# Optimization experiments

Measured on AMD Instinct MI355X. Metric: run time of the kernel, lower is better.

Reference implementation:

```python
import jax, jax.numpy as jnp
import numpy as np

H = 50  # hidden size

def _lstm_last_h(x, W_ih, W_hh, b_ih, b_hh):
    """Run a single-layer LSTM (PyTorch gate order i,f,g,o) over x [B,T,1],
    return final hidden state h_T [B,H]. Zero initial (h, c)."""
    B = x.shape[0]
    h0 = jnp.zeros((B, H), dtype=x.dtype)
    c0 = jnp.zeros((B, H), dtype=x.dtype)
    b = b_ih + b_hh  # [4H]

    def step(carry, xt):
        h, c = carry
        # gates: [B,4H]
        gates = xt @ W_ih.T + h @ W_hh.T + b
        i, f, g, o = jnp.split(gates, 4, axis=-1)
        i = jax.nn.sigmoid(i)
        f = jax.nn.sigmoid(f)
        g = jnp.tanh(g)
        o = jax.nn.sigmoid(o)
        c = f * c + i * g
        h = o * jnp.tanh(c)
        return (h, c), None

    xt = jnp.swapaxes(x, 0, 1)  # [T,B,1]
    (hT, _), _ = jax.lax.scan(step, (h0, c0), xt)
    return hT


def setup_inputs() -> dict:
    key = jax.random.key(0)
    ks = jax.random.split(key, 7)
    B, T = 1024, 96
    s = 1.0 / np.sqrt(H)  # PyTorch LSTM init scale
    return {
        "x": jax.random.normal(ks[0], (B, T, 1), dtype=jnp.float32),
        "W_ih": jax.random.uniform(ks[1], (4 * H, 1), jnp.float32, -s, s),
        "W_hh": jax.random.uniform(ks[2], (4 * H, H), jnp.float32, -s, s),
        "b_ih": jax.random.uniform(ks[3], (4 * H,), jnp.float32, -s, s),
        "b_hh": jax.random.uniform(ks[4], (4 * H,), jnp.float32, -s, s),
        "W_fc": jax.random.uniform(ks[5], (1, H), jnp.float32, -s, s),
        "b_fc": jax.random.uniform(ks[6], (1,), jnp.float32, -s, s),
        "num_pred": 12,
    }


def reference(x, W_ih, W_hh, b_ih, b_hh, W_fc, b_fc, num_pred):
    preds = []
    for _ in range(num_pred):  # static loop over prediction horizon
        hT = _lstm_last_h(x, W_ih, W_hh, b_ih, b_hh)        # [B,H]
        out = hT @ W_fc.T + b_fc                            # [B,1]
        preds.append(out[:, 0])
        # append prediction as next input, drop oldest timestep (window slides)
        x = jnp.concatenate([x, out[:, :, None]], axis=1)[:, 1:, :]
    return jnp.stack(preds, axis=1)  # [B, num_pred]
```

## Files before the change

kernel.cpp:

```cpp
#include <hip/hip_runtime.h>
#include <stdint.h>


#define HSZ 50
#define TLEN 96

#define GRP(WT,A0,A1,A2,A3,IL,IH,FL,FH,GL,GH,OL,OH,BL,BH,POST) \
    "s_waitcnt lgkmcnt(" WT ")\n\t" \
    "v_pk_fma_f32 v[" A0 "], v[" IL "], v[" BL "], v[" A0 "]\n\t" \
    "v_pk_fma_f32 v[" A1 "], v[" FL "], v[" BL "], v[" A1 "]\n\t" \
    "v_pk_fma_f32 v[" A2 "], v[" GL "], v[" BL "], v[" A2 "]\n\t" \
    "v_pk_fma_f32 v[" A3 "], v[" OL "], v[" BL "], v[" A3 "]\n\t" \
    "v_pk_fma_f32 v[" A0 "], v[" IH "], v[" BH "], v[" A0 "]\n\t" \
    "v_pk_fma_f32 v[" A1 "], v[" FH "], v[" BH "], v[" A1 "]\n\t" \
    "v_pk_fma_f32 v[" A2 "], v[" GH "], v[" BH "], v[" A2 "]\n\t" \
    "v_pk_fma_f32 v[" A3 "], v[" OH "], v[" BH "], v[" A3 "]\n\t" \
    POST
#define GRPM(WT,A0,A1,A2,A3,IL,IH,FL,FH,GL,GH,OL,OH,BL,BH,POST) \
    "s_waitcnt lgkmcnt(" WT ")\n\t" \
    "v_pk_mul_f32 v[" A0 "], v[" IL "], v[" BL "]\n\t" \
    "v_pk_mul_f32 v[" A1 "], v[" FL "], v[" BL "]\n\t" \
    "v_pk_mul_f32 v[" A2 "], v[" GL "], v[" BL "]\n\t" \
    "v_pk_mul_f32 v[" A3 "], v[" OL "], v[" BL "]\n\t" \
    "v_pk_fma_f32 v[" A0 "], v[" IH "], v[" BH "], v[" A0 "]\n\t" \
    "v_pk_fma_f32 v[" A1 "], v[" FH "], v[" BH "], v[" A1 "]\n\t" \
    "v_pk_fma_f32 v[" A2 "], v[" GH "], v[" BH "], v[" A2 "]\n\t" \
    "v_pk_fma_f32 v[" A3 "], v[" OH "], v[" BH "], v[" A3 "]\n\t" \
    POST
#define GRPX(...)  GRP(__VA_ARGS__)
#define GRPMX(...) GRPM(__VA_ARGS__)

#define ACC "28:29","30:31","32:33","34:35"
#define W0  "48:49","50:51","100:101","102:103","152:153","154:155","204:205","206:207"
#define W1  "52:53","54:55","104:105","106:107","156:157","158:159","208:209","210:211"
#define W2  "56:57","58:59","108:109","110:111","160:161","162:163","212:213","214:215"
#define W3  "60:61","62:63","112:113","114:115","164:165","166:167","216:217","218:219"
#define W4  "64:65","66:67","116:117","118:119","168:169","170:171","220:221","222:223"
#define W5  "68:69","70:71","120:121","122:123","172:173","174:175","224:225","226:227"
#define W6  "72:73","74:75","124:125","126:127","176:177","178:179","228:229","230:231"
#define W7  "76:77","78:79","128:129","130:131","180:181","182:183","232:233","234:235"
#define W8  "80:81","82:83","132:133","134:135","184:185","186:187","236:237","238:239"
#define W9  "84:85","86:87","136:137","138:139","188:189","190:191","240:241","242:243"
#define W10 "88:89","90:91","140:141","142:143","192:193","194:195","244:245","246:247"
#define W11 "92:93","94:95","144:145","146:147","196:197","198:199","248:249","250:251"
#define W12 "96:97","98:99","148:149","150:151","200:201","202:203","252:253","254:255"
#define SL0 "0:1","2:3"
#define SL1 "4:5","6:7"
#define SL2 "8:9","10:11"
#define SL3 "12:13","14:15"
#define SL4 "16:17","18:19"
#define SL5 "20:21","22:23"
#define SL6 "24:25","26:27"

__global__ __attribute__((amdgpu_flat_work_group_size(64, 64),
                          amdgpu_waves_per_eu(1, 1)))
void rec_lstm_kernel(const float* __restrict__ x,
                     const float* __restrict__ W_ih,
                     const float* __restrict__ W_hh,
                     const float* __restrict__ b_ih,
                     const float* __restrict__ b_hh,
                     const float* __restrict__ W_fc,
                     const float* __restrict__ b_fc,
                     const int*   __restrict__ num_pred,
                     float*       __restrict__ out)
{
    const int b = blockIdx.x;
    const int j = threadIdx.x;

    __shared__ __align__(16) float lds[176];
    if (j < 48) { lds[64 + j] = x[b*TLEN + j]; lds[64 + j + 48] = x[b*TLEN + j + 48]; }

    const int NP = num_pred[0];
    const uint32_t lb = (uint32_t)(uintptr_t)&lds[0];

    asm volatile(
        "s_load_dword s25, %[bfcp], 0x0\n\t"
        "s_waitcnt lgkmcnt(0)\n\t"
        "v_mbcnt_lo_u32_b32 v0, -1, 0\n\t"
        "v_mbcnt_hi_u32_b32 v0, -1, v0\n\t"
        "s_mov_b32 s22, 49\n\t"
        "v_min_u32 v1, s22, v0\n\t"
        "s_mov_b32 s22, 200\n\t"
        "v_mul_lo_u32 v2, s22, v1\n\t"
        "s_mov_b32 s22, 10000\n\t"
        "v_add_u32 v3, s22, v2\n\t"
        "s_mov_b32 s22, 20000\n\t"
        "v_add_u32 v4, s22, v2\n\t"
        "s_mov_b32 s22, 30000\n\t"
        "v_add_u32 v5, s22, v2\n\t"
        "v_lshlrev_b32 v6, 2, v1\n\t"
        "global_load_dword v48,  v6, %[bih]\n\t"
        "global_load_dword v100, v6, %[bih] offset:200\n\t"
        "global_load_dword v152, v6, %[bih] offset:400\n\t"
        "global_load_dword v204, v6, %[bih] offset:600\n\t"
        "global_load_dword v7,  v6, %[bhh]\n\t"
        "global_load_dword v8,  v6, %[bhh] offset:200\n\t"
        "global_load_dword v9,  v6, %[bhh] offset:400\n\t"
        "global_load_dword v10, v6, %[bhh] offset:600\n\t"
        "global_load_dword v49,  v6, %[wih]\n\t"
        "global_load_dword v101, v6, %[wih] offset:200\n\t"
        "global_load_dword v153, v6, %[wih] offset:400\n\t"
        "global_load_dword v205, v6, %[wih] offset:600\n\t"
        "global_load_dword v41, v6, %[wfcp]\n\t"
        "global_load_dwordx4 v[50:53], v2, %[whh]\n\t"
        "global_load_dwordx4 v[54:57], v2, %[whh] offset:16\n\t"
        "global_load_dwordx4 v[58:61], v2, %[whh] offset:32\n\t"
        "global_load_dwordx4 v[62:65], v2, %[whh] offset:48\n\t"
        "global_load_dwordx4 v[66:69], v2, %[whh] offset:64\n\t"
        "global_load_dwordx4 v[70:73], v2, %[whh] offset:80\n\t"
        "global_load_dwordx4 v[74:77], v2, %[whh] offset:96\n\t"
        "global_load_dwordx4 v[78:81], v2, %[whh] offset:112\n\t"
        "global_load_dwordx4 v[82:85], v2, %[whh] offset:128\n\t"
        "global_load_dwordx4 v[86:89], v2, %[whh] offset:144\n\t"
        "global_load_dwordx4 v[90:93], v2, %[whh] offset:160\n\t"
        "global_load_dwordx4 v[94:97], v2, %[whh] offset:176\n\t"
        "global_load_dwordx2 v[98:99], v2, %[whh] offset:192\n\t"
        "global_load_dwordx4 v[102:105], v3, %[whh]\n\t"
        "global_load_dwordx4 v[106:109], v3, %[whh] offset:16\n\t"
        "global_load_dwordx4 v[110:113], v3, %[whh] offset:32\n\t"
        "global_load_dwordx4 v[114:117], v3, %[whh] offset:48\n\t"
        "global_load_dwordx4 v[118:121], v3, %[whh] offset:64\n\t"
        "global_load_dwordx4 v[122:125], v3, %[whh] offset:80\n\t"
        "global_load_dwordx4 v[126:129], v3, %[whh] offset:96\n\t"
        "global_load_dwordx4 v[130:133], v3, %[whh] offset:112\n\t"
        "global_load_dwordx4 v[134:137], v3, %[whh] offset:128\n\t"
        "global_load_dwordx4 v[138:141], v3, %[whh] offset:144\n\t"
        "global_load_dwordx4 v[142:145], v3, %[whh] offset:160\n\t"
        "global_load_dwordx4 v[146:149], v3, %[whh] offset:176\n\t"
        "global_load_dwordx2 v[150:151], v3, %[whh] offset:192\n\t"
        "global_load_dwordx4 v[154:157], v4, %[whh]\n\t"
        "global_load_dwordx4 v[158:161], v4, %[whh] offset:16\n\t"
        "global_load_dwordx4 v[162:165], v4, %[whh] offset:32\n\t"
        "global_load_dwordx4 v[166:169], v4, %[whh] offset:48\n\t"
        "global_load_dwordx4 v[170:173], v4, %[whh] offset:64\n\t"
        "global_load_dwordx4 v[174:177], v4, %[whh] offset:80\n\t"
        "global_load_dwordx4 v[178:181], v4, %[whh] offset:96\n\t"
        "global_load_dwordx4 v[182:185], v4, %[whh] offset:112\n\t"
        "global_load_dwordx4 v[186:189], v4, %[whh] offset:128\n\t"
        "global_load_dwordx4 v[190:193], v4, %[whh] offset:144\n\t"
        "global_load_dwordx4 v[194:197], v4, %[whh] offset:160\n\t"
        "global_load_dwordx4 v[198:201], v4, %[whh] offset:176\n\t"
        "global_load_dwordx2 v[202:203], v4, %[whh] offset:192\n\t"
        "global_load_dwordx4 v[206:209], v5, %[whh]\n\t"
        "global_load_dwordx4 v[210:213], v5, %[whh] offset:16\n\t"
        "global_load_dwordx4 v[214:217], v5, %[whh] offset:32\n\t"
        "global_load_dwordx4 v[218:221], v5, %[whh] offset:48\n\t"
        "global_load_dwordx4 v[222:225], v5, %[whh] offset:64\n\t"
        "global_load_dwordx4 v[226:229], v5, %[whh] offset:80\n\t"
        "global_load_dwordx4 v[230:233], v5, %[whh] offset:96\n\t"
        "global_load_dwordx4 v[234:237], v5, %[whh] offset:112\n\t"
        "global_load_dwordx4 v[238:241], v5, %[whh] offset:128\n\t"
        "global_load_dwordx4 v[242:245], v5, %[whh] offset:144\n\t"
        "global_load_dwordx4 v[246:249], v5, %[whh] offset:160\n\t"
        "global_load_dwordx4 v[250:253], v5, %[whh] offset:176\n\t"
        "global_load_dwordx2 v[254:255], v5, %[whh] offset:192\n\t"
        "s_waitcnt vmcnt(0)\n\t"
        "v_add_f32 v48,  v48,  v7\n\t"
        "v_add_f32 v100, v100, v8\n\t"
        "v_add_f32 v152, v152, v9\n\t"
        "v_add_f32 v204, v204, v10\n\t"
        "v_cmp_gt_u32 vcc, 50, v0\n\t"
        "v_cndmask_b32 v41, 0, v41, vcc\n\t"
        "v_mov_b32 v38, %[lb]\n\t"
        "v_lshl_add_u32 v39, v1, 2, v38\n\t"
        "v_add_u32 v39, 8, v39\n\t"
        "v_add_u32 v40, 0x100, v38\n\t"
        "v_mov_b32 v44, 1.0\n\t"
        "ds_write_b32 v38, v44\n\t"
        "s_mov_b32 s21, %[np]\n\t"
        "4:\n\t"
        "v_mov_b32 v36, 0\n\t"
        "v_mov_b32 v44, 0\n\t"
        "ds_write_b32 v39, v44\n\t"
        "ds_read_b32 v42, v40\n\t"
        "s_waitcnt lgkmcnt(0)\n\t"
        "ds_write_b32 v38, v42 offset:4\n\t"
        "ds_read_b128 v[0:3],   v38 offset:0\n\t"
        "ds_read_b128 v[4:7],   v38 offset:16\n\t"
        "ds_read_b128 v[8:11],  v38 offset:32\n\t"
        "ds_read_b128 v[12:15], v38 offset:48\n\t"
        "ds_read_b128 v[16:19], v38 offset:64\n\t"
        "ds_read_b128 v[20:23], v38 offset:80\n\t"
        "ds_read_b128 v[24:27], v38 offset:96\n\t"
        "s_mov_b32 s20, 96\n\t"
        "3:\n\t"
        "ds_read_b32 v42, v40 offset:4\n\t"
        GRPMX("7", ACC, W0,  SL0, "ds_read_b128 v[0:3],   v38 offset:112\n\t")
        GRPX("7",  ACC, W1,  SL1, "ds_read_b128 v[4:7],   v38 offset:128\n\t")
        GRPX("7",  ACC, W2,  SL2, "ds_read_b128 v[8:11],  v38 offset:144\n\t")
        GRPX("7",  ACC, W3,  SL3, "ds_read_b128 v[12:15], v38 offset:160\n\t")
        GRPX("7",  ACC, W4,  SL4, "ds_read_b128 v[16:19], v38 offset:176\n\t")
        GRPX("7",  ACC, W5,  SL5, "ds_read_b128 v[20:23], v38 offset:192\n\t")
        GRPX("7",  ACC, W6,  SL6, "")
        GRPX("5",  ACC, W7,  SL0, "")
        GRPX("4",  ACC, W8,  SL1, "")
        GRPX("3",  ACC, W9,  SL2, "")
        GRPX("2",  ACC, W10, SL3, "")
        GRPX("1",  ACC, W11, SL4, "")
        GRPX("0",  ACC, W12, SL5, "")
        "v_add_f32 v28, v28, v29\n\t"
        "v_add_f32 v30, v30, v31\n\t"
        "v_add_f32 v32, v32, v33\n\t"
        "v_add_f32 v34, v34, v35\n\t"
        "v_mul_f32 v29, 0xbfb8aa3b, v28\n\t"
        "v_mul_f32 v31, 0xbfb8aa3b, v30\n\t"
        "v_mul_f32 v33, 0x4038aa3b, v32\n\t"
        "v_mul_f32 v35, 0xbfb8aa3b, v34\n\t"
        "v_exp_f32 v29, v29\n\t"
        "v_exp_f32 v31, v31\n\t"
        "v_exp_f32 v33, v33\n\t"
        "v_exp_f32 v35, v35\n\t"
        "v_add_f32 v29, 1.0, v29\n\t"
        "v_add_f32 v31, 1.0, v31\n\t"
        "v_add_f32 v33, 1.0, v33\n\t"
        "v_add_f32 v35, 1.0, v35\n\t"
        "v_rcp_f32 v29, v29\n\t"
        "v_rcp_f32 v31, v31\n\t"
        "v_rcp_f32 v33, v33\n\t"
        "v_rcp_f32 v35, v35\n\t"
        "s_nop 1\n\t"
        "v_fma_f32 v33, -2.0, v33, 1.0\n\t"
        "v_mul_f32 v29, v29, v33\n\t"
        "v_fma_f32 v36, v31, v36, v29\n\t"
        "v_mul_f32 v31, 0x4038aa3b, v36\n\t"
        "v_exp_f32 v31, v31\n\t"
        "s_nop 1\n\t"
        "v_add_f32 v31, 1.0, v31\n\t"
        "v_rcp_f32 v31, v31\n\t"
        "s_nop 1\n\t"
        "v_fma_f32 v31, -2.0, v31, 1.0\n\t"
        "v_mul_f32 v37, v35, v31\n\t"
        "ds_write_b32 v39, v37\n\t"
        "ds_write_b32 v38, v42 offset:4\n\t"
        "ds_read_b128 v[0:3],   v38 offset:0\n\t"
        "ds_read_b128 v[4:7],   v38 offset:16\n\t"
        "ds_read_b128 v[8:11],  v38 offset:32\n\t"
        "ds_read_b128 v[12:15], v38 offset:48\n\t"
        "ds_read_b128 v[16:19], v38 offset:64\n\t"
        "ds_read_b128 v[20:23], v38 offset:80\n\t"
        "ds_read_b128 v[24:27], v38 offset:96\n\t"
        "v_add_u32 v40, 4, v40\n\t"
        "s_sub_u32 s20, s20, 1\n\t"
        "s_cmp_lg_u32 s20, 0\n\t"
        "s_cbranch_scc1 3b\n\t"
        "v_mul_f32 v44, v37, v41\n\t"
        "s_nop 1\n\t"
        "ds_swizzle_b32 v45, v44 offset:0x041F\n\t"
        "s_waitcnt lgkmcnt(0)\n\t"
        "v_add_f32 v44, v44, v45\n\t"
        "ds_swizzle_b32 v45, v44 offset:0x081F\n\t"
        "s_waitcnt lgkmcnt(0)\n\t"
        "v_add_f32 v44, v44, v45\n\t"
        "ds_swizzle_b32 v45, v44 offset:0x101F\n\t"
        "s_waitcnt lgkmcnt(0)\n\t"
        "v_add_f32 v44, v44, v45\n\t"
        "ds_swizzle_b32 v45, v44 offset:0x201F\n\t"
        "s_waitcnt lgkmcnt(0)\n\t"
        "v_add_f32 v44, v44, v45\n\t"
        "ds_swizzle_b32 v45, v44 offset:0x401F\n\t"
        "s_waitcnt lgkmcnt(0)\n\t"
        "v_add_f32 v44, v44, v45\n\t"
        "s_nop 1\n\t"
        "v_readlane_b32 s26, v44, 0\n\t"
        "v_readlane_b32 s27, v44, 32\n\t"
        "s_nop 4\n\t"
        "v_mov_b32 v45, s26\n\t"
        "v_add_f32 v45, s27, v45\n\t"
        "v_add_f32 v45, s25, v45\n\t"
        "ds_write_b32 v40, v45\n\t"
        "s_waitcnt lgkmcnt(0)\n\t"
        "v_add_u32 v40, 0xfffffe84, v40\n\t"
        "s_sub_u32 s21, s21, 1\n\t"
        "s_cmp_lg_u32 s21, 0\n\t"
        "s_cbranch_scc1 4b\n\t"
        :
        : [lb] "v"(lb), [np] "s"(NP),
          [whh] "s"(W_hh), [wih] "s"(W_ih), [bih] "s"(b_ih), [bhh] "s"(b_hh),
          [wfcp] "s"(W_fc), [bfcp] "s"(b_fc)
        : "memory", "scc", "vcc", "s20", "s21", "s22", "s25", "s26", "s27",
          "v0","v1","v2","v3","v4","v5","v6","v7","v8","v9","v10","v11",
          "v12","v13","v14","v15","v16","v17","v18","v19","v20","v21","v22",
          "v23","v24","v25","v26","v27","v28","v29","v30","v31","v32","v33",
          "v34","v35","v36","v37","v38","v39","v40","v41","v42","v43","v44",
          "v45",
          "v48","v49","v50","v51","v52","v53","v54","v55","v56","v57","v58",
          "v59","v60","v61","v62","v63","v64","v65","v66","v67","v68","v69",
          "v70","v71","v72","v73","v74","v75","v76","v77","v78","v79","v80",
          "v81","v82","v83","v84","v85","v86","v87","v88","v89","v90","v91",
          "v92","v93","v94","v95","v96","v97","v98","v99","v100","v101",
          "v102","v103","v104","v105","v106","v107","v108","v109","v110",
          "v111","v112","v113","v114","v115","v116","v117","v118","v119",
          "v120","v121","v122","v123","v124","v125","v126","v127","v128",
          "v129","v130","v131","v132","v133","v134","v135","v136","v137",
          "v138","v139","v140","v141","v142","v143","v144","v145","v146",
          "v147","v148","v149","v150","v151","v152","v153","v154","v155",
          "v156","v157","v158","v159","v160","v161","v162","v163","v164",
          "v165","v166","v167","v168","v169","v170","v171","v172","v173",
          "v174","v175","v176","v177","v178","v179","v180","v181","v182",
          "v183","v184","v185","v186","v187","v188","v189","v190","v191",
          "v192","v193","v194","v195","v196","v197","v198","v199","v200",
          "v201","v202","v203","v204","v205","v206","v207","v208","v209",
          "v210","v211","v212","v213","v214","v215","v216","v217","v218",
          "v219","v220","v221","v222","v223","v224","v225","v226","v227",
          "v228","v229","v230","v231","v232","v233","v234","v235","v236",
          "v237","v238","v239","v240","v241","v242","v243","v244","v245",
          "v246","v247","v248","v249","v250","v251","v252","v253","v254",
          "v255");

    if (j < NP) out[b * NP + j] = lds[64 + TLEN + j];
}

extern "C" void kernel_launch(void* const* d_in, const int* in_sizes, int n_in,
                              void* d_out, int out_size, void* d_ws, size_t ws_size,
                              hipStream_t stream)
{
    const float* x    = (const float*)d_in[0];
    const float* W_ih = (const float*)d_in[1];
    const float* W_hh = (const float*)d_in[2];
    const float* b_ih = (const float*)d_in[3];
    const float* b_hh = (const float*)d_in[4];
    const float* W_fc = (const float*)d_in[5];
    const float* b_fc = (const float*)d_in[6];
    const int*   np   = (const int*)d_in[7];
    float* out = (float*)d_out;

    const int B = in_sizes[0] / TLEN;
    rec_lstm_kernel<<<B, 64, 0, stream>>>(x, W_ih, W_hh, b_ih, b_hh,
                                          W_fc, b_fc, np, out);
}
```

Baseline: 501.4 us.

## Pipeline alternating prediction horizons across two waves with LDS flag handoff

Launches two waves per block. Each wave handles every other prediction of the autoregressive horizon. A wave starts the next window's LSTM scan straight away and waits on a per-prediction LDS flag only before the last timestep, which is the one that needs the previous wave's output. This overlaps almost all of consecutive 96-step recurrences that previously ran back to back. In exchange it adds a spin-wait, relies on 2 waves per EU fitting 256 VGPRs each, shrinks the LDS prefetch buffering, and assumes an even num_pred.

```diff
diff --git a/kernel.cpp b/kernel.cpp
--- a/kernel.cpp
+++ b/kernel.cpp
@@ -2,35 +2,33 @@
 #include <stdint.h>
 
 
-#define HSZ 50
 #define TLEN 96
 
-#define GRP(WT,A0,A1,A2,A3,IL,IH,FL,FH,GL,GH,OL,OH,BL,BH,POST) \
+#define GRP(WT,IL,IH,FL,FH,GL,GH,OL,OH,BL,BH,POST) \
     "s_waitcnt lgkmcnt(" WT ")\n\t" \
-    "v_pk_fma_f32 v[" A0 "], v[" IL "], v[" BL "], v[" A0 "]\n\t" \
-    "v_pk_fma_f32 v[" A1 "], v[" FL "], v[" BL "], v[" A1 "]\n\t" \
-    "v_pk_fma_f32 v[" A2 "], v[" GL "], v[" BL "], v[" A2 "]\n\t" \
-    "v_pk_fma_f32 v[" A3 "], v[" OL "], v[" BL "], v[" A3 "]\n\t" \
-    "v_pk_fma_f32 v[" A0 "], v[" IH "], v[" BH "], v[" A0 "]\n\t" \
-    "v_pk_fma_f32 v[" A1 "], v[" FH "], v[" BH "], v[" A1 "]\n\t" \
-    "v_pk_fma_f32 v[" A2 "], v[" GH "], v[" BH "], v[" A2 "]\n\t" \
-    "v_pk_fma_f32 v[" A3 "], v[" OH "], v[" BH "], v[" A3 "]\n\t" \
+    "v_pk_fma_f32 v[16:17], v[" IL "], v[" BL "], v[16:17]\n\t" \
+    "v_pk_fma_f32 v[18:19], v[" FL "], v[" BL "], v[18:19]\n\t" \
+    "v_pk_fma_f32 v[20:21], v[" GL "], v[" BL "], v[20:21]\n\t" \
+    "v_pk_fma_f32 v[22:23], v[" OL "], v[" BL "], v[22:23]\n\t" \
+    "v_pk_fma_f32 v[16:17], v[" IH "], v[" BH "], v[16:17]\n\t" \
+    "v_pk_fma_f32 v[18:19], v[" FH "], v[" BH "], v[18:19]\n\t" \
+    "v_pk_fma_f32 v[20:21], v[" GH "], v[" BH "], v[20:21]\n\t" \
+    "v_pk_fma_f32 v[22:23], v[" OH "], v[" BH "], v[22:23]\n\t" \
     POST
-#define GRPM(WT,A0,A1,A2,A3,IL,IH,FL,FH,GL,GH,OL,OH,BL,BH,POST) \
+#define GRPM(WT,IL,IH,FL,FH,GL,GH,OL,OH,BL,BH,POST) \
     "s_waitcnt lgkmcnt(" WT ")\n\t" \
-    "v_pk_mul_f32 v[" A0 "], v[" IL "], v[" BL "]\n\t" \
-    "v_pk_mul_f32 v[" A1 "], v[" FL "], v[" BL "]\n\t" \
-    "v_pk_mul_f32 v[" A2 "], v[" GL "], v[" BL "]\n\t" \
-    "v_pk_mul_f32 v[" A3 "], v[" OL "], v[" BL "]\n\t" \
-    "v_pk_fma_f32 v[" A0 "], v[" IH "], v[" BH "], v[" A0 "]\n\t" \
-    "v_pk_fma_f32 v[" A1 "], v[" FH "], v[" BH "], v[" A1 "]\n\t" \
-    "v_pk_fma_f32 v[" A2 "], v[" GH "], v[" BH "], v[" A2 "]\n\t" \
-    "v_pk_fma_f32 v[" A3 "], v[" OH "], v[" BH "], v[" A3 "]\n\t" \
+    "v_pk_mul_f32 v[16:17], v[" IL "], v[" BL "]\n\t" \
+    "v_pk_mul_f32 v[18:19], v[" FL "], v[" BL "]\n\t" \
+    "v_pk_mul_f32 v[20:21], v[" GL "], v[" BL "]\n\t" \
+    "v_pk_mul_f32 v[22:23], v[" OL "], v[" BL "]\n\t" \
+    "v_pk_fma_f32 v[16:17], v[" IH "], v[" BH "], v[16:17]\n\t" \
+    "v_pk_fma_f32 v[18:19], v[" FH "], v[" BH "], v[18:19]\n\t" \
+    "v_pk_fma_f32 v[20:21], v[" GH "], v[" BH "], v[20:21]\n\t" \
+    "v_pk_fma_f32 v[22:23], v[" OH "], v[" BH "], v[22:23]\n\t" \
     POST
 #define GRPX(...)  GRP(__VA_ARGS__)
 #define GRPMX(...) GRPM(__VA_ARGS__)
 
-#define ACC "28:29","30:31","32:33","34:35"
 #define W0  "48:49","50:51","100:101","102:103","152:153","154:155","204:205","206:207"
 #define W1  "52:53","54:55","104:105","106:107","156:157","158:159","208:209","210:211"
 #define W2  "56:57","58:59","108:109","110:111","160:161","162:163","212:213","214:215"
@@ -48,12 +46,9 @@
 #define SL1 "4:5","6:7"
 #define SL2 "8:9","10:11"
 #define SL3 "12:13","14:15"
-#define SL4 "16:17","18:19"
-#define SL5 "20:21","22:23"
-#define SL6 "24:25","26:27"
-
-__global__ __attribute__((amdgpu_flat_work_group_size(64, 64),
-                          amdgpu_waves_per_eu(1, 1)))
+
+__global__ __attribute__((amdgpu_flat_work_group_size(128, 128),
+                          amdgpu_waves_per_eu(2)))
 void rec_lstm_kernel(const float* __restrict__ x,
                      const float* __restrict__ W_ih,
                      const float* __restrict__ W_hh,
@@ -64,14 +59,21 @@
                      const int*   __restrict__ num_pred,
                      float*       __restrict__ out)
 {
-    const int b = blockIdx.x;
-    const int j = threadIdx.x;
-
-    __shared__ __align__(16) float lds[176];
-    if (j < 48) { lds[64 + j] = x[b*TLEN + j]; lds[64 + j + 48] = x[b*TLEN + j + 48]; }
-
+    const int b   = blockIdx.x;
+    const int tid = threadIdx.x;
+
+    __shared__ __align__(16) float lds[256];
+    if (tid < TLEN) lds[128 + tid] = x[b * TLEN + tid];
+    if (tid < 16)  ((uint32_t*)lds)[240 + tid] = (tid == 0) ? 1u : 0u;
     const int NP = num_pred[0];
-    const uint32_t lb = (uint32_t)(uintptr_t)&lds[0];
+    __syncthreads();
+
+    const int      wid = tid >> 6;
+    const uint32_t lb  = (uint32_t)(uintptr_t)&lds[0];
+    const uint32_t hb  = lb + 256u * (uint32_t)wid;
+    const uint32_t xa0 = lb + 512u + 4u * (uint32_t)wid;
+    const uint32_t fa0 = lb + 960u + 4u * (uint32_t)wid;
+    const int      np2 = NP >> 1;
 
     asm volatile(
         "s_load_dword s25, %[bfcp], 0x0\n\t"
@@ -101,7 +103,7 @@
         "global_load_dword v101, v6, %[wih] offset:200\n\t"
         "global_load_dword v153, v6, %[wih] offset:400\n\t"
         "global_load_dword v205, v6, %[wih] offset:600\n\t"
-        "global_load_dword v41, v6, %[wfcp]\n\t"
+        "global_load_dword v29, v6, %[wfcp]\n\t"
         "global_load_dwordx4 v[50:53], v2, %[whh]\n\t"
         "global_load_dwordx4 v[54:57], v2, %[whh] offset:16\n\t"
         "global_load_dwordx4 v[58:61], v2, %[whh] offset:32\n\t"
@@ -160,129 +162,134 @@
         "v_add_f32 v152, v152, v9\n\t"
         "v_add_f32 v204, v204, v10\n\t"
         "v_cmp_gt_u32 vcc, 50, v0\n\t"
-        "v_cndmask_b32 v41, 0, v41, vcc\n\t"
-        "v_mov_b32 v38, %[lb]\n\t"
-        "v_lshl_add_u32 v39, v1, 2, v38\n\t"
-        "v_add_u32 v39, 8, v39\n\t"
-        "v_add_u32 v40, 0x100, v38\n\t"
-        "v_mov_b32 v44, 1.0\n\t"
-        "ds_write_b32 v38, v44\n\t"
-        "s_mov_b32 s21, %[np]\n\t"
+        "v_cndmask_b32 v29, 0, v29, vcc\n\t"
+        "v_mov_b32 v26, %[hb]\n\t"
+        "v_lshl_add_u32 v27, v1, 2, v26\n\t"
+        "v_add_u32 v27, 8, v27\n\t"
+        "v_mov_b32 v28, %[xa0]\n\t"
+        "v_mov_b32 v33, %[fa0]\n\t"
+        "v_mov_b32 v31, 1.0\n\t"
+        "ds_write_b32 v26, v31\n\t"
+        "s_mov_b32 s21, %[np2]\n\t"
         "4:\n\t"
-        "v_mov_b32 v36, 0\n\t"
-        "v_mov_b32 v44, 0\n\t"
-        "ds_write_b32 v39, v44\n\t"
-        "ds_read_b32 v42, v40\n\t"
-        "s_waitcnt lgkmcnt(0)\n\t"
-        "ds_write_b32 v38, v42 offset:4\n\t"
-        "ds_read_b128 v[0:3],   v38 offset:0\n\t"
-        "ds_read_b128 v[4:7],   v38 offset:16\n\t"
-        "ds_read_b128 v[8:11],  v38 offset:32\n\t"
-        "ds_read_b128 v[12:15], v38 offset:48\n\t"
-        "ds_read_b128 v[16:19], v38 offset:64\n\t"
-        "ds_read_b128 v[20:23], v38 offset:80\n\t"
-        "ds_read_b128 v[24:27], v38 offset:96\n\t"
+        "v_mov_b32 v24, 0\n\t"
+        "v_mov_b32 v31, 0\n\t"
+        "ds_write_b32 v27, v31\n\t"
+        "ds_read_b32 v30, v28\n\t"
+        "s_waitcnt lgkmcnt(0)\n\t"
+        "ds_write_b32 v26, v30 offset:4\n\t"
+        "ds_read_b128 v[0:3],   v26 offset:0\n\t"
+        "ds_read_b128 v[4:7],   v26 offset:16\n\t"
+        "ds_read_b128 v[8:11],  v26 offset:32\n\t"
+        "ds_read_b128 v[12:15], v26 offset:48\n\t"
         "s_mov_b32 s20, 96\n\t"
         "3:\n\t"
-        "ds_read_b32 v42, v40 offset:4\n\t"
-        GRPMX("7", ACC, W0,  SL0, "ds_read_b128 v[0:3],   v38 offset:112\n\t")
-        GRPX("7",  ACC, W1,  SL1, "ds_read_b128 v[4:7],   v38 offset:128\n\t")
-        GRPX("7",  ACC, W2,  SL2, "ds_read_b128 v[8:11],  v38 offset:144\n\t")
-        GRPX("7",  ACC, W3,  SL3, "ds_read_b128 v[12:15], v38 offset:160\n\t")
-        GRPX("7",  ACC, W4,  SL4, "ds_read_b128 v[16:19], v38 offset:176\n\t")
-        GRPX("7",  ACC, W5,  SL5, "ds_read_b128 v[20:23], v38 offset:192\n\t")
-        GRPX("7",  ACC, W6,  SL6, "")
-        GRPX("5",  ACC, W7,  SL0, "")
-        GRPX("4",  ACC, W8,  SL1, "")
-        GRPX("3",  ACC, W9,  SL2, "")
-        GRPX("2",  ACC, W10, SL3, "")
-        GRPX("1",  ACC, W11, SL4, "")
-        GRPX("0",  ACC, W12, SL5, "")
-        "v_add_f32 v28, v28, v29\n\t"
-        "v_add_f32 v30, v30, v31\n\t"
-        "v_add_f32 v32, v32, v33\n\t"
-        "v_add_f32 v34, v34, v35\n\t"
-        "v_mul_f32 v29, 0xbfb8aa3b, v28\n\t"
-        "v_mul_f32 v31, 0xbfb8aa3b, v30\n\t"
-        "v_mul_f32 v33, 0x4038aa3b, v32\n\t"
-        "v_mul_f32 v35, 0xbfb8aa3b, v34\n\t"
-        "v_exp_f32 v29, v29\n\t"
-        "v_exp_f32 v31, v31\n\t"
-        "v_exp_f32 v33, v33\n\t"
-        "v_exp_f32 v35, v35\n\t"
-        "v_add_f32 v29, 1.0, v29\n\t"
-        "v_add_f32 v31, 1.0, v31\n\t"
-        "v_add_f32 v33, 1.0, v33\n\t"
-        "v_add_f32 v35, 1.0, v35\n\t"
-        "v_rcp_f32 v29, v29\n\t"
-        "v_rcp_f32 v31, v31\n\t"
-        "v_rcp_f32 v33, v33\n\t"
-        "v_rcp_f32 v35, v35\n\t"
-        "s_nop 1\n\t"
-        "v_fma_f32 v33, -2.0, v33, 1.0\n\t"
-        "v_mul_f32 v29, v29, v33\n\t"
-        "v_fma_f32 v36, v31, v36, v29\n\t"
-        "v_mul_f32 v31, 0x4038aa3b, v36\n\t"
-        "v_exp_f32 v31, v31\n\t"
-        "s_nop 1\n\t"
-        "v_add_f32 v31, 1.0, v31\n\t"
-        "v_rcp_f32 v31, v31\n\t"
-        "s_nop 1\n\t"
-        "v_fma_f32 v31, -2.0, v31, 1.0\n\t"
-        "v_mul_f32 v37, v35, v31\n\t"
-        "ds_write_b32 v39, v37\n\t"
-        "ds_write_b32 v38, v42 offset:4\n\t"
-        "ds_read_b128 v[0:3],   v38 offset:0\n\t"
-        "ds_read_b128 v[4:7],   v38 offset:16\n\t"
-        "ds_read_b128 v[8:11],  v38 offset:32\n\t"
-        "ds_read_b128 v[12:15], v38 offset:48\n\t"
-        "ds_read_b128 v[16:19], v38 offset:64\n\t"
-        "ds_read_b128 v[20:23], v38 offset:80\n\t"
-        "ds_read_b128 v[24:27], v38 offset:96\n\t"
-        "v_add_u32 v40, 4, v40\n\t"
+        "s_cmp_lg_u32 s20, 2\n\t"
+        "s_cbranch_scc1 31f\n\t"
+        "30:\n\t"
+        "ds_read_b32 v34, v33\n\t"
+        "s_waitcnt lgkmcnt(0)\n\t"
+        "v_cmp_ne_u32 vcc, 0, v34\n\t"
+        "s_cbranch_vccz 30b\n\t"
+        "31:\n\t"
+        "ds_read_b32 v30, v28 offset:4\n\t"
+        GRPMX("4", W0,  SL0, "ds_read_b128 v[0:3],   v26 offset:64\n\t")
+        GRPX("4",  W1,  SL1, "ds_read_b128 v[4:7],   v26 offset:80\n\t")
+        GRPX("4",  W2,  SL2, "ds_read_b128 v[8:11],  v26 offset:96\n\t")
+        GRPX("4",  W3,  SL3, "ds_read_b128 v[12:15], v26 offset:112\n\t")
+        GRPX("3",  W4,  SL0, "ds_read_b128 v[0:3],   v26 offset:128\n\t")
+        GRPX("3",  W5,  SL1, "ds_read_b128 v[4:7],   v26 offset:144\n\t")
+        GRPX("3",  W6,  SL2, "ds_read_b128 v[8:11],  v26 offset:160\n\t")
+        GRPX("3",  W7,  SL3, "ds_read_b128 v[12:15], v26 offset:176\n\t")
+        GRPX("3",  W8,  SL0, "ds_read_b128 v[0:3],   v26 offset:192\n\t")
+        GRPX("3",  W9,  SL1, "")
+        GRPX("2",  W10, SL2, "")
+        GRPX("1",  W11, SL3, "")
+        GRPX("0",  W12, SL0, "")
+        "v_add_f32 v16, v16, v17\n\t"
+        "v_add_f32 v18, v18, v19\n\t"
+        "v_add_f32 v20, v20, v21\n\t"
+        "v_add_f32 v22, v22, v23\n\t"
+        "v_mul_f32 v17, 0xbfb8aa3b, v16\n\t"
+        "v_mul_f32 v19, 0xbfb8aa3b, v18\n\t"
+        "v_mul_f32 v21, 0x4038aa3b, v20\n\t"
+        "v_mul_f32 v23, 0xbfb8aa3b, v22\n\t"
+        "v_exp_f32 v17, v17\n\t"
+        "v_exp_f32 v19, v19\n\t"
+        "v_exp_f32 v21, v21\n\t"
+        "v_exp_f32 v23, v23\n\t"
+        "v_add_f32 v17, 1.0, v17\n\t"
+        "v_add_f32 v19, 1.0, v19\n\t"
+        "v_add_f32 v21, 1.0, v21\n\t"
+        "v_add_f32 v23, 1.0, v23\n\t"
+        "v_rcp_f32 v17, v17\n\t"
+        "v_rcp_f32 v19, v19\n\t"
+        "v_rcp_f32 v21, v21\n\t"
+        "v_rcp_f32 v23, v23\n\t"
+        "s_nop 1\n\t"
+        "v_fma_f32 v21, -2.0, v21, 1.0\n\t"
+        "v_mul_f32 v17, v17, v21\n\t"
+        "v_fma_f32 v24, v19, v24, v17\n\t"
+        "v_mul_f32 v19, 0x4038aa3b, v24\n\t"
+        "v_exp_f32 v19, v19\n\t"
+        "s_nop 1\n\t"
+        "v_add_f32 v19, 1.0, v19\n\t"
+        "v_rcp_f32 v19, v19\n\t"
+        "s_nop 1\n\t"
+        "v_fma_f32 v19, -2.0, v19, 1.0\n\t"
+        "v_mul_f32 v25, v23, v19\n\t"
+        "ds_write_b32 v27, v25\n\t"
+        "ds_write_b32 v26, v30 offset:4\n\t"
+        "ds_read_b128 v[0:3],   v26 offset:0\n\t"
+        "ds_read_b128 v[4:7],   v26 offset:16\n\t"
+        "ds_read_b128 v[8:11],  v26 offset:32\n\t"
+        "ds_read_b128 v[12:15], v26 offset:48\n\t"
+        "v_add_u32 v28, 4, v28\n\t"
         "s_sub_u32 s20, s20, 1\n\t"
         "s_cmp_lg_u32 s20, 0\n\t"
         "s_cbranch_scc1 3b\n\t"
-        "v_mul_f32 v44, v37, v41\n\t"
-        "s_nop 1\n\t"
-        "ds_swizzle_b32 v45, v44 offset:0x041F\n\t"
-        "s_waitcnt lgkmcnt(0)\n\t"
-        "v_add_f32 v44, v44, v45\n\t"
-        "ds_swizzle_b32 v45, v44 offset:0x081F\n\t"
-        "s_waitcnt lgkmcnt(0)\n\t"
-        "v_add_f32 v44, v44, v45\n\t"
-        "ds_swizzle_b32 v45, v44 offset:0x101F\n\t"
-        "s_waitcnt lgkmcnt(0)\n\t"
-        "v_add_f32 v44, v44, v45\n\t"
-        "ds_swizzle_b32 v45, v44 offset:0x201F\n\t"
-        "s_waitcnt lgkmcnt(0)\n\t"
-        "v_add_f32 v44, v44, v45\n\t"
-        "ds_swizzle_b32 v45, v44 offset:0x401F\n\t"
-        "s_waitcnt lgkmcnt(0)\n\t"
-        "v_add_f32 v44, v44, v45\n\t"
-        "s_nop 1\n\t"
-        "v_readlane_b32 s26, v44, 0\n\t"
-        "v_readlane_b32 s27, v44, 32\n\t"
+        "v_mul_f32 v31, v25, v29\n\t"
+        "s_nop 1\n\t"
+        "ds_swizzle_b32 v32, v31 offset:0x041F\n\t"
+        "s_waitcnt lgkmcnt(0)\n\t"
+        "v_add_f32 v31, v31, v32\n\t"
+        "ds_swizzle_b32 v32, v31 offset:0x081F\n\t"
+        "s_waitcnt lgkmcnt(0)\n\t"
+        "v_add_f32 v31, v31, v32\n\t"
+        "ds_swizzle_b32 v32, v31 offset:0x101F\n\t"
+        "s_waitcnt lgkmcnt(0)\n\t"
+        "v_add_f32 v31, v31, v32\n\t"
+        "ds_swizzle_b32 v32, v31 offset:0x201F\n\t"
+        "s_waitcnt lgkmcnt(0)\n\t"
+        "v_add_f32 v31, v31, v32\n\t"
+        "ds_swizzle_b32 v32, v31 offset:0x401F\n\t"
+        "s_waitcnt lgkmcnt(0)\n\t"
+        "v_add_f32 v31, v31, v32\n\t"
+        "s_nop 1\n\t"
+        "v_readlane_b32 s26, v31, 0\n\t"
+        "v_readlane_b32 s27, v31, 32\n\t"
         "s_nop 4\n\t"
-        "v_mov_b32 v45, s26\n\t"
-        "v_add_f32 v45, s27, v45\n\t"
-        "v_add_f32 v45, s25, v45\n\t"
-        "ds_write_b32 v40, v45\n\t"
-        "s_waitcnt lgkmcnt(0)\n\t"
-        "v_add_u32 v40, 0xfffffe84, v40\n\t"
+        "v_mov_b32 v32, s26\n\t"
+        "v_add_f32 v32, s27, v32\n\t"
+        "v_add_f32 v32, s25, v32\n\t"
+        "ds_write_b32 v28, v32\n\t"
+        "v_mov_b32 v34, 1.0\n\t"
+        "ds_write_b32 v33, v34 offset:4\n\t"
+        "s_waitcnt lgkmcnt(0)\n\t"
+        "v_add_u32 v28, 0xfffffe88, v28\n\t"
+        "v_add_u32 v33, 8, v33\n\t"
         "s_sub_u32 s21, s21, 1\n\t"
         "s_cmp_lg_u32 s21, 0\n\t"
         "s_cbranch_scc1 4b\n\t"
         :
-        : [lb] "v"(lb), [np] "s"(NP),
+        : [hb] "v"(hb), [xa0] "v"(xa0), [fa0] "v"(fa0), [np2] "s"(np2),
           [whh] "s"(W_hh), [wih] "s"(W_ih), [bih] "s"(b_ih), [bhh] "s"(b_hh),
           [wfcp] "s"(W_fc), [bfcp] "s"(b_fc)
         : "memory", "scc", "vcc", "s20", "s21", "s22", "s25", "s26", "s27",
           "v0","v1","v2","v3","v4","v5","v6","v7","v8","v9","v10","v11",
           "v12","v13","v14","v15","v16","v17","v18","v19","v20","v21","v22",
           "v23","v24","v25","v26","v27","v28","v29","v30","v31","v32","v33",
-          "v34","v35","v36","v37","v38","v39","v40","v41","v42","v43","v44",
-          "v45",
+          "v34",
           "v48","v49","v50","v51","v52","v53","v54","v55","v56","v57","v58",
           "v59","v60","v61","v62","v63","v64","v65","v66","v67","v68","v69",
           "v70","v71","v72","v73","v74","v75","v76","v77","v78","v79","v80",
@@ -307,7 +314,8 @@
           "v246","v247","v248","v249","v250","v251","v252","v253","v254",
           "v255");
 
-    if (j < NP) out[b * NP + j] = lds[64 + TLEN + j];
+    __syncthreads();
+    if (tid < NP) out[b * NP + tid] = lds[224 + tid];
 }
 
 extern "C" void kernel_launch(void* const* d_in, const int* in_sizes, int n_in,
@@ -325,6 +333,6 @@
     float* out = (float*)d_out;
 
     const int B = in_sizes[0] / TLEN;
-    rec_lstm_kernel<<<B, 64, 0, stream>>>(x, W_ih, W_hh, b_ih, b_hh,
-                                          W_fc, b_fc, np, out);
+    rec_lstm_kernel<<<B, 128, 0, stream>>>(x, W_ih, W_hh, b_ih, b_hh,
+                                           W_fc, b_fc, np, out);
 }
```

Result: faster. 448.7 us (-10.5%).
